# Kernel optimization log

Measured on AMD Instinct MI355X. Metric: run time of the kernel, lower is better.

The kernel has to match this reference:

```python
import jax, jax.numpy as jnp
import numpy as np
import math

NEG_INF = -1e9  # large negative used as masked-logit value (pre-scaling, as in the original)


def setup_inputs() -> dict:
    key = jax.random.key(0)
    k1, k2, k3 = jax.random.split(key, 3)
    bs, ql, kl, d = 8, 2048, 2048, 512
    return {
        "query": jax.random.normal(k1, (bs, ql, d), dtype=jnp.float32),
        "key": jax.random.normal(k2, (bs, kl, d), dtype=jnp.float32),
        "value": jax.random.normal(k3, (bs, kl, d), dtype=jnp.float32),
        "use_mask": 1,
        "cell_dim": 512,
    }


def reference(query, key, value, use_mask, cell_dim):
    bs, ql, d = query.shape[0], query.shape[1], value.shape[2]
    kl = key.shape[1]
    # [bs, ql, kl] raw scores
    mm = jnp.einsum("bqd,bkd->bqk", query, key)
    if use_mask:
        # mask positions where key index > query index (strictly future)
        q_idx = jnp.arange(ql)[:, None]
        k_idx = jnp.arange(kl)[None, :]
        mask = (k_idx > q_idx).astype(mm.dtype)  # [ql, kl]
        mm = mm + mask[None, :, :] * NEG_INF
    # log_softmax(...).exp() == softmax, computed stably in one pass
    w = jax.nn.softmax(mm / math.sqrt(cell_dim), axis=2)
    # weighted value aggregation (original broadcasts to [bs,ql,kl,d]; einsum fuses it)
    res = jnp.einsum("bqk,bkd->bqd", w, value)
    return res
```

## Files before the change

### kernel.cpp

```cpp
#include <hip/hip_runtime.h>
#include <math.h>

typedef __bf16 bf16x8 __attribute__((ext_vector_type(8)));
typedef float floatx4 __attribute__((ext_vector_type(4)));
typedef unsigned short ushort8_t __attribute__((ext_vector_type(8)));

#define BSZ 8
#define SEQ 2048
#define DIM 512
#define BKEY 32
#define BQ 128

__device__ __forceinline__ unsigned short f2bf(float f) {
    unsigned int u = __float_as_uint(f);
    u += 0x7fffu + ((u >> 16) & 1u);
    return (unsigned short)(u >> 16);
}
__device__ __forceinline__ float bf2f(unsigned short s) {
    return __uint_as_float(((unsigned int)s) << 16);
}

#define ASYNC16(g, l) __builtin_amdgcn_global_load_lds( \
    (const __attribute__((address_space(1))) unsigned int*)(g), \
    (__attribute__((address_space(3))) unsigned int*)(l), 16, 0, 0)

__global__ __launch_bounds__(256) void prep_kv(const float* __restrict__ K,
                                               const float* __restrict__ V,
                                               unsigned short* __restrict__ Kb,
                                               unsigned short* __restrict__ Vt) {
    if (blockIdx.x < 4096) {
        size_t i = ((size_t)blockIdx.x * 256 + threadIdx.x) * 8;
        float4 a = *(const float4*)(K + i);
        float4 b = *(const float4*)(K + i + 4);
        ushort8_t u;
        u[0]=f2bf(a.x); u[1]=f2bf(a.y); u[2]=f2bf(a.z); u[3]=f2bf(a.w);
        u[4]=f2bf(b.x); u[5]=f2bf(b.y); u[6]=f2bf(b.z); u[7]=f2bf(b.w);
        *(ushort8_t*)(Kb + i) = u;
        return;
    }
    __shared__ unsigned short T[BKEY][DIM + 8];
    const int bid = blockIdx.x - 4096;
    const int b = bid & 7, kb = bid >> 3;
    const float* src = V + ((size_t)b * SEQ + (size_t)kb * BKEY) * DIM;
    const int tid = threadIdx.x;
    #pragma unroll
    for (int i = 0; i < 16; ++i) {
        const int idx = i * 256 + tid;
        const int key = idx >> 7;
        const int d = (idx & 127) * 4;
        float4 x = *(const float4*)(src + (size_t)key * DIM + d);
        T[key][d]   = f2bf(x.x);
        T[key][d+1] = f2bf(x.y);
        T[key][d+2] = f2bf(x.z);
        T[key][d+3] = f2bf(x.w);
    }
    __syncthreads();
    unsigned short* dst = Vt + (size_t)(b * (SEQ / BKEY) + kb) * DIM * BKEY;
    #pragma unroll
    for (int i = 0; i < 8; ++i) {
        const int cidx = i * 256 + tid;
        const int d = cidx >> 2;
        const int kc = cidx & 3;
        ushort8_t v;
        #pragma unroll
        for (int k2 = 0; k2 < 8; ++k2) v[k2] = T[kc * 8 + k2][d];
        *(ushort8_t*)(dst + cidx * 8) = v;
    }
}


template <int SPLIT, int CH, int NSLOT>
__global__ __launch_bounds__(512, 2)
void attn_fwd(const float* __restrict__ Q,
              const unsigned short* __restrict__ Kb,
              const unsigned short* __restrict__ Vt,
              unsigned short* __restrict__ PartO,
              float* __restrict__ Pml,
              float* __restrict__ O)
{
    __shared__ unsigned short Ksh[2][BKEY * DIM];
    __shared__ unsigned short Vsh[2][DIM * BKEY];
    __shared__ unsigned short Psh[8 * 16 * BKEY];

    const int tid  = threadIdx.x;
    const int lane = tid & 63;
    const int wv   = tid >> 6;
    const int ml   = lane & 15;
    const int quad = lane >> 4;

    const int bid = blockIdx.x;
    const int b   = bid & 7;
    const int j   = bid >> 3;
    int t, c;
    if (SPLIT) {
        t = 15; c = j;
        while (true) { const int cnt = (4 * t + 4 + CH - 1) / CH; if (c < cnt) break; c -= cnt; --t; }
    } else { t = 15 - j; c = 0; }
    const int nk  = 4 * t + 4;
    const int kt0 = c * CH;
    const int kt1 = SPLIT ? min(kt0 + CH, nk) : nk;
    const bool is_split = SPLIT && (nk > CH);
    const int q0 = t * BQ;
    const int kdiag = 4 * t;

    const float* Qb = Q + (size_t)b * SEQ * DIM;
    const unsigned short* Kbb = Kb + (size_t)b * SEQ * DIM;
    const unsigned short* Vtb = Vt + (size_t)b * SEQ * DIM;
    float* Ob = O + (size_t)b * SEQ * DIM;

    bf16x8 qf[16];
    {
        const float* qp = Qb + (size_t)(q0 + wv * 16 + ml) * DIM + quad * 8;
        #pragma unroll
        for (int kc = 0; kc < 16; ++kc) {
            float4 x = *(const float4*)(qp + kc * 32);
            float4 y = *(const float4*)(qp + kc * 32 + 4);
            union { bf16x8 v; unsigned short s[8]; } u;
            u.s[0]=f2bf(x.x); u.s[1]=f2bf(x.y); u.s[2]=f2bf(x.z); u.s[3]=f2bf(x.w);
            u.s[4]=f2bf(y.x); u.s[5]=f2bf(y.y); u.s[6]=f2bf(y.z); u.s[7]=f2bf(y.w);
            qf[kc] = u.v;
        }
    }
    asm volatile("" ::: "memory");

    floatx4 acc[32];
    #pragma unroll
    for (int i = 0; i < 32; ++i) acc[i] = (floatx4){0.f, 0.f, 0.f, 0.f};
    float mrun[4] = {-1e30f, -1e30f, -1e30f, -1e30f};
    float lrun[4] = {0.f, 0.f, 0.f, 0.f};

    const float CS = 1.4426950408889634f * 0.04419417382415922f;

    #define STAGE_K(buf_, kt_) do { \
        const unsigned short* Kt_ = Kbb + (size_t)(kt_) * (BKEY * DIM); \
        unsigned short* Kd_ = &Ksh[(buf_)][0]; \
        _Pragma("unroll") \
        for (int i_ = 0; i_ < 4; ++i_) { \
            const int ci_  = i_ * 512 + tid; \
            const int row_ = ci_ >> 6; \
            const int ch_  = (ci_ & 63) ^ (row_ & 7); \
            ASYNC16(Kt_ + (size_t)row_ * DIM + ch_ * 8, Kd_ + ci_ * 8); \
        } } while (0)
    #define STAGE_V(buf_, kt_) do { \
        const unsigned short* Vt_ = Vtb + (size_t)(kt_) * (DIM * BKEY); \
        unsigned short* Vd_ = &Vsh[(buf_)][0]; \
        _Pragma("unroll") \
        for (int i_ = 0; i_ < 4; ++i_) { \
            const int ci_ = i_ * 512 + tid; \
            const int d_  = ci_ >> 2; \
            const int kc_ = (ci_ & 3) ^ (d_ & 3); \
            ASYNC16(Vt_ + d_ * BKEY + kc_ * 8, Vd_ + ci_ * 8); \
        } } while (0)

    STAGE_K(0, kt0);
    STAGE_V(0, kt0);
    asm volatile("s_waitcnt vmcnt(4)" ::: "memory");
    __builtin_amdgcn_s_barrier();

    int cur = 0;
    for (int kt = kt0; kt < kt1; ++kt) {
        const int k0 = kt * BKEY;
        const bool havenxt = (kt + 1 < kt1);

        if (havenxt) STAGE_K(cur ^ 1, kt + 1);

        const unsigned short* Ks = &Ksh[cur][0];
        floatx4 s0 = (floatx4){0,0,0,0}, s1 = (floatx4){0,0,0,0};
        floatx4 s0b = (floatx4){0,0,0,0}, s1b = (floatx4){0,0,0,0};
        const int sw = ml & 7;
        __builtin_amdgcn_s_setprio(1);
        #pragma unroll
        for (int kc = 0; kc < 16; kc += 2) {
            const int ch0 = kc * 4 + quad, ch1 = (kc + 1) * 4 + quad;
            bf16x8 a0 = *(bf16x8*)&Ks[ml * DIM + ((ch0 ^ sw) << 3)];
            bf16x8 a1 = *(bf16x8*)&Ks[(16 + ml) * DIM + ((ch0 ^ sw) << 3)];
            bf16x8 b0 = *(bf16x8*)&Ks[ml * DIM + ((ch1 ^ sw) << 3)];
            bf16x8 b1 = *(bf16x8*)&Ks[(16 + ml) * DIM + ((ch1 ^ sw) << 3)];
            s0  = __builtin_amdgcn_mfma_f32_16x16x32_bf16(qf[kc],     a0, s0,  0, 0, 0);
            s1  = __builtin_amdgcn_mfma_f32_16x16x32_bf16(qf[kc],     a1, s1,  0, 0, 0);
            s0b = __builtin_amdgcn_mfma_f32_16x16x32_bf16(qf[kc + 1], b0, s0b, 0, 0, 0);
            s1b = __builtin_amdgcn_mfma_f32_16x16x32_bf16(qf[kc + 1], b1, s1b, 0, 0, 0);
        }
        __builtin_amdgcn_s_setprio(0);
        s0 = s0 + s0b;
        s1 = s1 + s1b;

        if (kt >= kdiag) {
            #pragma unroll
            for (int r = 0; r < 4; ++r) {
                const int qg = q0 + wv * 16 + quad * 4 + r;
                s0[r] = (k0 + ml > qg)      ? -INFINITY : s0[r] * CS;
                s1[r] = (k0 + 16 + ml > qg) ? -INFINITY : s1[r] * CS;
            }
        } else {
            #pragma unroll
            for (int r = 0; r < 4; ++r) { s0[r] *= CS; s1[r] *= CS; }
        }

        float al[4];
        #pragma unroll
        for (int r = 0; r < 4; ++r) {
            float v = fmaxf(s0[r], s1[r]);
            v = fmaxf(v, __shfl_xor(v, 1, 64));
            v = fmaxf(v, __shfl_xor(v, 2, 64));
            v = fmaxf(v, __shfl_xor(v, 4, 64));
            v = fmaxf(v, __shfl_xor(v, 8, 64));
            const float d = v - mrun[r];
            const bool up = d > 8.0f;
            al[r]   = up ? __builtin_amdgcn_exp2f(-d) : 1.0f;
            mrun[r] = up ? v : mrun[r];
        }
        #pragma unroll
        for (int r = 0; r < 4; ++r) {
            s0[r] = __builtin_amdgcn_exp2f(s0[r] - mrun[r]);
            s1[r] = __builtin_amdgcn_exp2f(s1[r] - mrun[r]);
            float rs = s0[r] + s1[r];
            rs += __shfl_xor(rs, 1, 64);
            rs += __shfl_xor(rs, 2, 64);
            rs += __shfl_xor(rs, 4, 64);
            rs += __shfl_xor(rs, 8, 64);
            lrun[r] = lrun[r] * al[r] + rs;
        }

        if (al[0] < 1.f || al[1] < 1.f || al[2] < 1.f || al[3] < 1.f) {
            #pragma unroll
            for (int nt = 0; nt < 32; ++nt) {
                acc[nt][0] *= al[0]; acc[nt][1] *= al[1];
                acc[nt][2] *= al[2]; acc[nt][3] *= al[3];
            }
        }

        unsigned short* Pw = &Psh[wv * (16 * BKEY)];
        #pragma unroll
        for (int r = 0; r < 4; ++r) {
            const int row = quad * 4 + r;
            const int col0 = ml;
            const int col1 = 16 + ml;
            Pw[row * BKEY + ((((col0 >> 3) ^ (row & 3)) << 3) | (col0 & 7))] = f2bf(s0[r]);
            Pw[row * BKEY + ((((col1 >> 3) ^ (row & 3)) << 3) | (col1 & 7))] = f2bf(s1[r]);
        }
        asm volatile("s_waitcnt lgkmcnt(0)" ::: "memory");
        bf16x8 pf = *(bf16x8*)&Pw[ml * BKEY + ((quad ^ (ml & 3)) << 3)];

        if (havenxt) { asm volatile("s_waitcnt vmcnt(4)" ::: "memory"); }
        else         { asm volatile("s_waitcnt vmcnt(0)" ::: "memory"); }
        __builtin_amdgcn_s_barrier();

        if (havenxt) STAGE_V(cur ^ 1, kt + 1);

        const unsigned short* Vs = &Vsh[cur][0];
        __builtin_amdgcn_s_setprio(1);
        #pragma unroll
        for (int nt = 0; nt < 32; ++nt) {
            const int drow = nt * 16 + ml;
            bf16x8 vf = *(bf16x8*)&Vs[drow * BKEY + ((quad ^ (drow & 3)) << 3)];
            acc[nt] = __builtin_amdgcn_mfma_f32_16x16x32_bf16(pf, vf, acc[nt], 0, 0, 0);
        }
        __builtin_amdgcn_s_setprio(0);

        if (havenxt) {
            asm volatile("s_waitcnt vmcnt(4)" ::: "memory");
            __builtin_amdgcn_s_barrier();
            cur ^= 1;
        }
    }
    #undef STAGE_K
    #undef STAGE_V

    if (!is_split) {
        float inv[4];
        #pragma unroll
        for (int r = 0; r < 4; ++r) inv[r] = 1.f / lrun[r];
        #pragma unroll
        for (int nt = 0; nt < 32; ++nt) {
            #pragma unroll
            for (int r = 0; r < 4; ++r) {
                const int row = q0 + wv * 16 + quad * 4 + r;
                Ob[(size_t)row * DIM + nt * 16 + ml] = acc[nt][r] * inv[r];
            }
        }
    } else {
        const size_t slot = (size_t)(b * NSLOT + j);
        unsigned short* po = PartO + slot * (BQ * DIM);
        #pragma unroll
        for (int nt = 0; nt < 32; ++nt) {
            #pragma unroll
            for (int r = 0; r < 4; ++r) {
                const int prow = wv * 16 + quad * 4 + r;
                po[prow * DIM + nt * 16 + ml] = f2bf(acc[nt][r]);
            }
        }
        if (ml == 0) {
            #pragma unroll
            for (int r = 0; r < 4; ++r) {
                const int prow = wv * 16 + quad * 4 + r;
                Pml[slot * 256 + prow * 2]     = mrun[r];
                Pml[slot * 256 + prow * 2 + 1] = lrun[r];
            }
        }
    }
}

template <int CH, int NSLOT, int TMIN>
__global__ __launch_bounds__(256)
void attn_merge(const unsigned short* __restrict__ PartO,
                const float* __restrict__ Pml,
                float* __restrict__ O)
{
    const int bid = blockIdx.x;
    const int b = bid & 7;
    const int u = bid >> 3;
    const int t = TMIN + (u >> 2);
    const int rg = u & 3;
    const int nc = (4 * t + 4 + CH - 1) / CH;
    int j0 = 0;
    for (int tp = 15; tp > t; --tp) j0 += (4 * tp + 4 + CH - 1) / CH;

    const int row = rg * 32 + (threadIdx.x >> 3);
    const int d0  = (threadIdx.x & 7) * 64;

    float M = -INFINITY;
    for (int cc = 0; cc < nc; ++cc) {
        const size_t slot = (size_t)(b * NSLOT + j0 + cc);
        M = fmaxf(M, Pml[slot * 256 + row * 2]);
    }
    float L = 0.f;
    for (int cc = 0; cc < nc; ++cc) {
        const size_t slot = (size_t)(b * NSLOT + j0 + cc);
        L += Pml[slot * 256 + row * 2 + 1] *
             __builtin_amdgcn_exp2f(Pml[slot * 256 + row * 2] - M);
    }

    float o[64];
    #pragma unroll
    for (int i = 0; i < 64; ++i) o[i] = 0.f;
    for (int cc = 0; cc < nc; ++cc) {
        const size_t slot = (size_t)(b * NSLOT + j0 + cc);
        const float w = __builtin_amdgcn_exp2f(Pml[slot * 256 + row * 2] - M);
        const unsigned short* po = PartO + slot * (BQ * DIM) + (size_t)row * DIM + d0;
        #pragma unroll
        for (int i = 0; i < 8; ++i) {
            ushort8_t v = *(const ushort8_t*)(po + i * 8);
            #pragma unroll
            for (int k2 = 0; k2 < 8; ++k2) o[i * 8 + k2] += w * bf2f(v[k2]);
        }
    }
    const float invL = 1.f / L;
    float* out = O + ((size_t)b * SEQ + (size_t)t * BQ + row) * DIM + d0;
    #pragma unroll
    for (int i = 0; i < 16; ++i) {
        float4 v4 = { o[i*4] * invL, o[i*4+1] * invL, o[i*4+2] * invL, o[i*4+3] * invL };
        *(float4*)(out + i * 4) = v4;
    }
}

extern "C" void kernel_launch(void* const* d_in, const int* in_sizes, int n_in,
                              void* d_out, int out_size, void* d_ws, size_t ws_size,
                              hipStream_t stream) {
    const float* Q = (const float*)d_in[0];
    const float* K = (const float*)d_in[1];
    const float* V = (const float*)d_in[2];
    float* Out = (float*)d_out;

    const size_t elems = (size_t)BSZ * SEQ * DIM;
    unsigned short* Kb = (unsigned short*)d_ws;
    unsigned short* Vt = Kb + elems;
    unsigned short* PartO = Vt + elems;
    const size_t kvbytes = 2 * elems * 2;

    prep_kv<<<dim3(4096 + BSZ * (SEQ / BKEY)), dim3(256), 0, stream>>>(K, V, Kb, Vt);

    const size_t need6 = kvbytes + (size_t)BSZ * 95 * BQ * DIM * 2 + (size_t)BSZ * 95 * 256 * 4;
    const size_t need8 = kvbytes + (size_t)BSZ * 70 * BQ * DIM * 2 + (size_t)BSZ * 70 * 256 * 4;

    if (ws_size >= need6) {
        float* Pml = (float*)(PartO + (size_t)BSZ * 95 * BQ * DIM);
        attn_fwd<1, 6, 95><<<dim3(BSZ * 96), dim3(512), 0, stream>>>(Q, Kb, Vt, PartO, Pml, Out);
        attn_merge<6, 95, 1><<<dim3(BSZ * 15 * 4), dim3(256), 0, stream>>>(PartO, Pml, Out);
    } else if (ws_size >= need8) {
        float* Pml = (float*)(PartO + (size_t)BSZ * 70 * BQ * DIM);
        attn_fwd<1, 8, 70><<<dim3(BSZ * 72), dim3(512), 0, stream>>>(Q, Kb, Vt, PartO, Pml, Out);
        attn_merge<8, 70, 2><<<dim3(BSZ * 14 * 4), dim3(256), 0, stream>>>(PartO, Pml, Out);
    } else {
        attn_fwd<0, 8, 70><<<dim3(BSZ * 16), dim3(512), 0, stream>>>(Q, Kb, Vt, PartO, (float*)PartO, Out);
    }
}
```

Baseline: 315.7 us.

## Prefetch V with K early and defer softmax row-sum reductions

Issues the next tile's V loads together with K at the top of each iteration, with wait counts adjusted, so V transfer overlaps the QK compute. Keeps per-lane partial row sums and reduces them once after the loop, and guards the max shuffles and accumulator rescale behind a wave-wide vote. This cuts cross-lane shuffle traffic per tile. It raises outstanding loads and makes the V buffer lifetime longer.

New measurement: 290.9 us. -7.8%, faster.

```diff
diff --git a/kernel.cpp b/kernel.cpp
--- a/kernel.cpp
+++ b/kernel.cpp
@@ -126,8 +126,8 @@
     floatx4 acc[32];
     #pragma unroll
     for (int i = 0; i < 32; ++i) acc[i] = (floatx4){0.f, 0.f, 0.f, 0.f};
-    float mrun[4] = {-1e30f, -1e30f, -1e30f, -1e30f};
-    float lrun[4] = {0.f, 0.f, 0.f, 0.f};
+    float mrun[4]  = {-1e30f, -1e30f, -1e30f, -1e30f};
+    float lpart[4] = {0.f, 0.f, 0.f, 0.f};
 
     const float CS = 1.4426950408889634f * 0.04419417382415922f;
 
@@ -162,7 +162,7 @@
         const int k0 = kt * BKEY;
         const bool havenxt = (kt + 1 < kt1);
 
-        if (havenxt) STAGE_K(cur ^ 1, kt + 1);
+        if (havenxt) { STAGE_K(cur ^ 1, kt + 1); STAGE_V(cur ^ 1, kt + 1); }
 
         const unsigned short* Ks = &Ksh[cur][0];
         floatx4 s0 = (floatx4){0,0,0,0}, s1 = (floatx4){0,0,0,0};
@@ -197,37 +197,41 @@
             for (int r = 0; r < 4; ++r) { s0[r] *= CS; s1[r] *= CS; }
         }
 
-        float al[4];
-        #pragma unroll
-        for (int r = 0; r < 4; ++r) {
-            float v = fmaxf(s0[r], s1[r]);
-            v = fmaxf(v, __shfl_xor(v, 1, 64));
-            v = fmaxf(v, __shfl_xor(v, 2, 64));
-            v = fmaxf(v, __shfl_xor(v, 4, 64));
-            v = fmaxf(v, __shfl_xor(v, 8, 64));
-            const float d = v - mrun[r];
-            const bool up = d > 8.0f;
-            al[r]   = up ? __builtin_amdgcn_exp2f(-d) : 1.0f;
-            mrun[r] = up ? v : mrun[r];
-        }
+        {
+            float pm[4];
+            bool need = false;
+            #pragma unroll
+            for (int r = 0; r < 4; ++r) {
+                pm[r] = fmaxf(s0[r], s1[r]);
+                need = need || (pm[r] > mrun[r] + 8.0f);
+            }
+            if (__any(need)) {
+                float al[4];
+                #pragma unroll
+                for (int r = 0; r < 4; ++r) {
+                    float v = pm[r];
+                    v = fmaxf(v, __shfl_xor(v, 1, 64));
+                    v = fmaxf(v, __shfl_xor(v, 2, 64));
+                    v = fmaxf(v, __shfl_xor(v, 4, 64));
+                    v = fmaxf(v, __shfl_xor(v, 8, 64));
+                    const float nm = fmaxf(mrun[r], v);
+                    al[r]   = __builtin_amdgcn_exp2f(mrun[r] - nm);
+                    mrun[r] = nm;
+                    lpart[r] *= al[r];
+                }
+                #pragma unroll
+                for (int nt = 0; nt < 32; ++nt) {
+                    acc[nt][0] *= al[0]; acc[nt][1] *= al[1];
+                    acc[nt][2] *= al[2]; acc[nt][3] *= al[3];
+                }
+            }
+        }
+
         #pragma unroll
         for (int r = 0; r < 4; ++r) {
             s0[r] = __builtin_amdgcn_exp2f(s0[r] - mrun[r]);
             s1[r] = __builtin_amdgcn_exp2f(s1[r] - mrun[r]);
-            float rs = s0[r] + s1[r];
-            rs += __shfl_xor(rs, 1, 64);
-            rs += __shfl_xor(rs, 2, 64);
-            rs += __shfl_xor(rs, 4, 64);
-            rs += __shfl_xor(rs, 8, 64);
-            lrun[r] = lrun[r] * al[r] + rs;
-        }
-
-        if (al[0] < 1.f || al[1] < 1.f || al[2] < 1.f || al[3] < 1.f) {
-            #pragma unroll
-            for (int nt = 0; nt < 32; ++nt) {
-                acc[nt][0] *= al[0]; acc[nt][1] *= al[1];
-                acc[nt][2] *= al[2]; acc[nt][3] *= al[3];
-            }
+            lpart[r] += s0[r] + s1[r];
         }
 
         unsigned short* Pw = &Psh[wv * (16 * BKEY)];
@@ -242,11 +246,9 @@
         asm volatile("s_waitcnt lgkmcnt(0)" ::: "memory");
         bf16x8 pf = *(bf16x8*)&Pw[ml * BKEY + ((quad ^ (ml & 3)) << 3)];
 
-        if (havenxt) { asm volatile("s_waitcnt vmcnt(4)" ::: "memory"); }
+        if (havenxt) { asm volatile("s_waitcnt vmcnt(8)" ::: "memory"); }
         else         { asm volatile("s_waitcnt vmcnt(0)" ::: "memory"); }
         __builtin_amdgcn_s_barrier();
-
-        if (havenxt) STAGE_V(cur ^ 1, kt + 1);
 
         const unsigned short* Vs = &Vsh[cur][0];
         __builtin_amdgcn_s_setprio(1);
@@ -266,6 +268,17 @@
     }
     #undef STAGE_K
     #undef STAGE_V
+
+    float lrun[4];
+    #pragma unroll
+    for (int r = 0; r < 4; ++r) {
+        float s = lpart[r];
+        s += __shfl_xor(s, 1, 64);
+        s += __shfl_xor(s, 2, 64);
+        s += __shfl_xor(s, 4, 64);
+        s += __shfl_xor(s, 8, 64);
+        lrun[r] = s;
+    }
 
     if (!is_split) {
         float inv[4];
```
